# Kernel optimization log

Hardware: AMD Instinct MI355X
Metric: run time of the kernel (lower is better)

Reference implementation:

```python
import jax, jax.numpy as jnp
import numpy as np

# YOLOv3 anchors (9 pairs, 3 per scale), matching init_kwargs
ANCHORS = np.array([[10,13],[16,30],[33,23],[30,61],[62,45],[59,119],[116,90],[156,198],[373,326]], dtype=np.float32)
B, C = 3, 20
IGNORE_THRESH = 0.7


def iou_xywh(a, b):
    """IoU of boxes in (cx,cy,w,h); a,b broadcastable [...,4]."""
    ax1, ax2 = a[..., 0] - a[..., 2] * 0.5, a[..., 0] + a[..., 2] * 0.5
    ay1, ay2 = a[..., 1] - a[..., 3] * 0.5, a[..., 1] + a[..., 3] * 0.5
    bx1, bx2 = b[..., 0] - b[..., 2] * 0.5, b[..., 0] + b[..., 2] * 0.5
    by1, by2 = b[..., 1] - b[..., 3] * 0.5, b[..., 1] + b[..., 3] * 0.5
    iw = jnp.clip(jnp.minimum(ax2, bx2) - jnp.maximum(ax1, bx1), 0.0)
    ih = jnp.clip(jnp.minimum(ay2, by2) - jnp.maximum(ay1, by1), 0.0)
    inter = iw * ih
    union = a[..., 2] * a[..., 3] + b[..., 2] * b[..., 3] - inter
    return inter / (union + 1e-16)


def _scale_loss(pred, targets, idx, img_size):
    anchors_total = jnp.asarray(ANCHORS)                      # [9,2]
    N = pred.shape[0]
    g = pred.shape[2]
    p = pred.reshape(N, B, C + 5, g, g).transpose(0, 1, 3, 4, 2)  # [N,B,g,g,C+5]
    xy = jax.nn.sigmoid(p[..., 0:2])
    wh = p[..., 2:4]                                          # raw tw,th
    conf = jax.nn.sigmoid(p[..., 4])
    pcls = jax.nn.sigmoid(p[..., 5:])

    yv, xv = jnp.meshgrid(jnp.arange(g), jnp.arange(g), indexing='ij')
    grid = jnp.stack([xv, yv], -1).astype(pred.dtype)[None, None]  # [1,1,g,g,2]
    a_wh = anchors_total[idx * B:(idx + 1) * B].reshape(1, B, 1, 1, 2)
    preds_coords = jnp.concatenate([(xy + grid) / g, jnp.exp(wh) * a_wh / img_size], -1)  # [N,B,g,g,4]

    tcls = targets[..., 0].astype(jnp.int32)                  # [N,T]
    tb = targets[..., 1:]                                     # [N,T,4]
    # break-on-first-zero-x semantics
    valid = jnp.cumprod((tb[..., 0] != 0).astype(jnp.int32), axis=1).astype(bool)

    # noobj mask: max IoU of every pred box vs every valid target
    ious = iou_xywh(preds_coords[:, None], tb[:, :, None, None, None])  # [N,T,B,g,g]
    ious = jnp.where(valid[:, :, None, None, None], ious, -1.0)
    noobj = ious.max(axis=1) <= IGNORE_THRESH                 # [N,B,g,g]

    # best-anchor matching (shift both to origin: only w,h matter)
    anc4 = jnp.concatenate([jnp.zeros_like(anchors_total), anchors_total / img_size], -1)  # [9,4]
    tb0 = tb.at[..., 0:2].set(0.0)
    a_ious = iou_xywh(anc4[None, None], tb0[:, :, None])      # [N,T,9]
    k = jnp.argmax(a_ious, axis=-1)                           # [N,T] global anchor idx
    matched = valid & (k // B == idx)
    local = k % B
    ii = jnp.clip(jnp.floor(tb[..., 0] * g), 0, g - 1).astype(jnp.int32)
    jj = jnp.clip(jnp.floor(tb[..., 1] * g), 0, g - 1).astype(jnp.int32)

    kwh = anchors_total[k]                                    # [N,T,2]
    tw_safe = jnp.maximum(tb[..., 2], 1e-12)                  # guard log(0) for padded rows (dropped anyway)
    th_safe = jnp.maximum(tb[..., 3], 1e-12)
    enc = jnp.stack([tb[..., 0] * g - ii,
                     tb[..., 1] * g - jj,
                     jnp.log(tw_safe * img_size / kwh[..., 0]),
                     jnp.log(th_safe * img_size / kwh[..., 1])], -1)  # [N,T,4]
    scale4 = jnp.broadcast_to((2.0 - tb[..., 2] * tb[..., 3])[..., None], enc.shape)

    b_idx = jnp.broadcast_to(jnp.arange(N)[:, None], matched.shape)
    b_s = jnp.where(matched, b_idx, N)                        # OOB batch idx -> dropped by scatter
    obj = jnp.zeros((N, B, g, g), bool).at[b_s, local, jj, ii].set(True, mode='drop')
    noobj = noobj.at[b_s, local, jj, ii].set(False, mode='drop')
    cls_t = jnp.zeros((N, B, g, g, C), pred.dtype).at[b_s, local, jj, ii, tcls].set(1.0, mode='drop')
    enc_t = jnp.zeros((N, B, g, g, 4), pred.dtype).at[b_s, local, jj, ii].set(enc, mode='drop')
    scl_t = jnp.zeros((N, B, g, g, 4), pred.dtype).at[b_s, local, jj, ii].set(scale4, mode='drop')

    loss_noobj = jnp.sum(jnp.where(noobj, conf, 0.0) ** 2)
    loss_obj = jnp.sum(jnp.where(obj, conf - 1.0, 0.0) ** 2)
    loss_class = jnp.sum(jnp.where(obj[..., None], pcls - cls_t, 0.0) ** 2)
    raw4 = jnp.concatenate([xy, wh], -1)
    diff = (raw4 - enc_t) * scl_t
    loss_coords = jnp.sum(jnp.where(obj[..., None], diff, 0.0) ** 2)
    return (loss_class + loss_obj + loss_noobj + loss_coords) / N


def setup_inputs() -> dict:
    key = jax.random.key(0)
    k0, k1, k2, k3, k4, k5, k6 = jax.random.split(key, 7)
    N, T = 16, 40
    pred0 = jax.random.normal(k0, (N, B * (C + 5), 19, 19), jnp.float32) * 0.5
    pred1 = jax.random.normal(k1, (N, B * (C + 5), 38, 38), jnp.float32) * 0.5
    pred2 = jax.random.normal(k2, (N, B * (C + 5), 76, 76), jnp.float32) * 0.5
    cls = jax.random.randint(k3, (N, T, 1), 0, C).astype(jnp.float32)
    xy = jax.random.uniform(k4, (N, T, 2), minval=0.05, maxval=0.95)
    wh = jax.random.uniform(k5, (N, T, 2), minval=0.02, maxval=0.4)
    counts = jax.random.randint(k6, (N, 1), 5, T + 1)
    mask = (jnp.arange(T)[None, :] < counts).astype(jnp.float32)[..., None]
    targets = jnp.concatenate([cls, xy, wh], -1) * mask  # zero padding tail -> break semantics
    return {"pred0": pred0, "pred1": pred1, "pred2": pred2, "targets": targets, "img_size": 608}


def reference(pred0, pred1, pred2, targets, img_size):
    return (_scale_loss(pred0, targets, 0, img_size)
            + _scale_loss(pred1, targets, 1, img_size)
            + _scale_loss(pred2, targets, 2, img_size))
```

## Files before the change

### kernel.cpp

```cpp
#include <hip/hip_runtime.h>

#define NB 16
#define TT 40
#define BA 3
#define CC 20

__constant__ float cANCH[18] = {10,13, 16,30, 33,23, 30,61, 62,45,
                                59,119, 116,90, 156,198, 373,326};

__device__ __forceinline__ float sigmoidf_(float x){ return 1.f/(1.f+__expf(-x)); }

__global__ __launch_bounds__(256) void yolo_loss_33457795236259_kernel(
    const float* __restrict__ p0, const float* __restrict__ p1,
    const float* __restrict__ p2, const float* __restrict__ targets,
    const void* __restrict__ imgp, float* __restrict__ out)
{
  const int n  = blockIdx.y;
  const int bx = blockIdx.x;
  int s, g, cellbase;
  const float* pred;
  if (bx < 5)       { s = 0; g = 19; pred = p0; cellbase = bx * 256; }
  else if (bx < 22) { s = 1; g = 38; pred = p1; cellbase = (bx - 5) * 256; }
  else              { s = 2; g = 76; pred = p2; cellbase = (bx - 22) * 256; }

  __shared__ float stx1[TT], stx2[TT], sty1[TT], sty2[TT], sarea[TT];
  __shared__ float senc0[TT], senc1[TT], senc2[TT], senc3[TT], sscl[TT];
  __shared__ int   smkey[TT];
  __shared__ int   scount;
  __shared__ float swsum[4];

  float img;
  { int v = *(const int*)imgp;
    img = (v >= 1 && v <= 1000000) ? (float)v : *(const float*)imgp; }

  const int tid = threadIdx.x;
  if (tid < TT) {
    const int t = tid;
    const float* tg = targets + (n * TT + t) * 5;
    float tcf = tg[0];
    float tx = tg[1], ty = tg[2], tw = tg[3], th = tg[4];
    bool valid = true;
    for (int u = 0; u <= t; ++u)
      if (targets[(n * TT + u) * 5 + 1] == 0.f) { valid = false; break; }
    stx1[t] = tx - tw * 0.5f; stx2[t] = tx + tw * 0.5f;
    sty1[t] = ty - th * 0.5f; sty2[t] = ty + th * 0.5f;
    sarea[t] = tw * th;
    sscl[t]  = 2.f - tw * th;
    int k = 0; float best = -1.f;
    for (int a = 0; a < 9; ++a) {
      float aw = cANCH[2*a] / img, ah = cANCH[2*a+1] / img;
      float inter = fminf(aw, tw) * fminf(ah, th);
      float uni   = aw * ah + tw * th - inter;
      float iou   = inter / (uni + 1e-16f);
      if (iou > best) { best = iou; k = a; }
    }
    float gf = (float)g;
    int ii = (int)floorf(tx * gf); ii = ii < 0 ? 0 : (ii > g-1 ? g-1 : ii);
    int jj = (int)floorf(ty * gf); jj = jj < 0 ? 0 : (jj > g-1 ? g-1 : jj);
    bool m = valid && (k / BA == s);
    int kl = k % BA;
    int tc = (int)tcf;
    smkey[t] = m ? (ii | (jj << 7) | (kl << 14) | (tc << 16)) : -1;
    senc0[t] = tx * gf - (float)ii;
    senc1[t] = ty * gf - (float)jj;
    senc2[t] = __logf(fmaxf(tw, 1e-12f) * img / cANCH[2*k]);
    senc3[t] = __logf(fmaxf(th, 1e-12f) * img / cANCH[2*k+1]);
    if (t == 0) {
      int cnt = 0;
      while (cnt < TT && targets[(n * TT + cnt) * 5 + 1] != 0.f) cnt++;
      scount = cnt;
    }
  }
  __syncthreads();

  float partial = 0.f;
  const int gg = g * g;
  const int cell = cellbase + tid;
  if (cell < BA * gg) {
    int b = cell / gg;
    int rem = cell - b * gg;
    int i = rem / g;
    int j = rem - i * g;
    const float* pc = pred + ((size_t)(n * BA + b) * (CC + 5)) * gg + rem;
    float rx = pc[0];
    float ry = pc[(size_t)gg];
    float rw = pc[(size_t)2 * gg];
    float rh = pc[(size_t)3 * gg];
    float rconf = pc[(size_t)4 * gg];
    float sx = sigmoidf_(rx), sy = sigmoidf_(ry), conf = sigmoidf_(rconf);
    float aw = cANCH[2*(s*BA+b)] / img, ah = cANCH[2*(s*BA+b)+1] / img;
    float pw = __expf(rw) * aw, ph = __expf(rh) * ah;
    float gf = (float)g;
    float cx = (sx + (float)j) / gf, cy = (sy + (float)i) / gf;
    float px1 = cx - pw * 0.5f, px2 = cx + pw * 0.5f;
    float py1 = cy - ph * 0.5f, py2 = cy + ph * 0.5f;
    float areaP = pw * ph;
    float maxiou = -1.f;
    int win = -1; unsigned clsmask = 0u;
    int mykey = j | (i << 7) | (b << 14);
    int cnt = scount;
    for (int t = 0; t < cnt; ++t) {
      float iw = fminf(px2, stx2[t]) - fmaxf(px1, stx1[t]);
      float ih = fminf(py2, sty2[t]) - fmaxf(py1, sty1[t]);
      iw = fmaxf(iw, 0.f); ih = fmaxf(ih, 0.f);
      float inter = iw * ih;
      float iou = inter / (areaP + sarea[t] - inter + 1e-16f);
      maxiou = fmaxf(maxiou, iou);
      int mk = smkey[t];
      if ((mk & 0xFFFF) == mykey) { win = t; clsmask |= 1u << (mk >> 16); }
    }
    if (win >= 0) {
      float d = conf - 1.f; partial += d * d;
      float scl = sscl[win];
      float d0 = (sx - senc0[win]) * scl;
      float d1 = (sy - senc1[win]) * scl;
      float d2 = (rw - senc2[win]) * scl;
      float d3 = (rh - senc3[win]) * scl;
      partial += d0*d0 + d1*d1 + d2*d2 + d3*d3;
      #pragma unroll
      for (int c = 0; c < CC; ++c) {
        float pcl = sigmoidf_(pc[(size_t)(5 + c) * gg]);
        float tv = ((clsmask >> c) & 1u) ? 1.f : 0.f;
        float dd = pcl - tv;
        partial += dd * dd;
      }
    } else if (maxiou <= 0.7f) {
      partial += conf * conf;
    }
  }

  #pragma unroll
  for (int o = 32; o >= 1; o >>= 1) partial += __shfl_down(partial, o, 64);
  int lane = tid & 63, wid = tid >> 6;
  if (lane == 0) swsum[wid] = partial;
  __syncthreads();
  if (tid == 0) {
    atomicAdd(out, (swsum[0] + swsum[1] + swsum[2] + swsum[3]) * (1.f / (float)NB));
  }
}

extern "C" void kernel_launch(void* const* d_in, const int* in_sizes, int n_in,
                              void* d_out, int out_size, void* d_ws, size_t ws_size,
                              hipStream_t stream) {
  const float* p0 = (const float*)d_in[0];
  const float* p1 = (const float*)d_in[1];
  const float* p2 = (const float*)d_in[2];
  const float* tg = (const float*)d_in[3];
  const void*  im = d_in[4];
  float* out = (float*)d_out;

  hipMemsetAsync(out, 0, sizeof(float), stream);

  dim3 grid(90, NB);
  yolo_loss_33457795236259_kernel<<<grid, 256, 0, stream>>>(p0, p1, p2, tg, im, out);
}
```

Before: 107.6 us.

## Replace atomic accumulation with per-block partials and a separate reduce kernel

Each block now writes its partial sum into a workspace array instead of doing an atomicAdd to the output, and a second single-block kernel reduces the partials. This drops the memset and the atomics and makes the sum deterministic, at the cost of an extra kernel launch. Target data in shared memory is packed into float4/float2 structs so the IoU loop issues fewer LDS instructions. The per-thread prefix validity scan is replaced by a single count computed before the target setup.

After: 102.1 us. -5.1%, faster.

```diff
diff --git a/kernel.cpp b/kernel.cpp
--- a/kernel.cpp
+++ b/kernel.cpp
@@ -4,16 +4,17 @@
 #define TT 40
 #define BA 3
 #define CC 20
+#define GX 90
 
 __constant__ float cANCH[18] = {10,13, 16,30, 33,23, 30,61, 62,45,
                                 59,119, 116,90, 156,198, 373,326};
 
 __device__ __forceinline__ float sigmoidf_(float x){ return 1.f/(1.f+__expf(-x)); }
 
-__global__ __launch_bounds__(256) void yolo_loss_33457795236259_kernel(
+__global__ __launch_bounds__(256) void yolo_part_kernel(
     const float* __restrict__ p0, const float* __restrict__ p1,
     const float* __restrict__ p2, const float* __restrict__ targets,
-    const void* __restrict__ imgp, float* __restrict__ out)
+    const void* __restrict__ imgp, float* __restrict__ partials)
 {
   const int n  = blockIdx.y;
   const int bx = blockIdx.x;
@@ -23,29 +24,33 @@
   else if (bx < 22) { s = 1; g = 38; pred = p1; cellbase = (bx - 5) * 256; }
   else              { s = 2; g = 76; pred = p2; cellbase = (bx - 22) * 256; }
 
-  __shared__ float stx1[TT], stx2[TT], sty1[TT], sty2[TT], sarea[TT];
-  __shared__ float senc0[TT], senc1[TT], senc2[TT], senc3[TT], sscl[TT];
-  __shared__ int   smkey[TT];
-  __shared__ int   scount;
-  __shared__ float swsum[4];
+  __shared__ float4 sbox[TT];
+  __shared__ float2 sai[TT];
+  __shared__ float4 sencv[TT];
+  __shared__ float  sscl[TT];
+  __shared__ int    scount;
+  __shared__ float  swsum[4];
 
   float img;
   { int v = *(const int*)imgp;
     img = (v >= 1 && v <= 1000000) ? (float)v : *(const float*)imgp; }
 
   const int tid = threadIdx.x;
+  if (tid == 0) {
+    int cnt = 0;
+    while (cnt < TT && targets[(n * TT + cnt) * 5 + 1] != 0.f) cnt++;
+    scount = cnt;
+  }
+  __syncthreads();
   if (tid < TT) {
     const int t = tid;
     const float* tg = targets + (n * TT + t) * 5;
     float tcf = tg[0];
     float tx = tg[1], ty = tg[2], tw = tg[3], th = tg[4];
-    bool valid = true;
-    for (int u = 0; u <= t; ++u)
-      if (targets[(n * TT + u) * 5 + 1] == 0.f) { valid = false; break; }
-    stx1[t] = tx - tw * 0.5f; stx2[t] = tx + tw * 0.5f;
-    sty1[t] = ty - th * 0.5f; sty2[t] = ty + th * 0.5f;
-    sarea[t] = tw * th;
-    sscl[t]  = 2.f - tw * th;
+    bool valid = t < scount;
+    sbox[t] = make_float4(tx - tw * 0.5f, tx + tw * 0.5f,
+                          ty - th * 0.5f, ty + th * 0.5f);
+    sscl[t] = 2.f - tw * th;
     int k = 0; float best = -1.f;
     for (int a = 0; a < 9; ++a) {
       float aw = cANCH[2*a] / img, ah = cANCH[2*a+1] / img;
@@ -60,16 +65,11 @@
     bool m = valid && (k / BA == s);
     int kl = k % BA;
     int tc = (int)tcf;
-    smkey[t] = m ? (ii | (jj << 7) | (kl << 14) | (tc << 16)) : -1;
-    senc0[t] = tx * gf - (float)ii;
-    senc1[t] = ty * gf - (float)jj;
-    senc2[t] = __logf(fmaxf(tw, 1e-12f) * img / cANCH[2*k]);
-    senc3[t] = __logf(fmaxf(th, 1e-12f) * img / cANCH[2*k+1]);
-    if (t == 0) {
-      int cnt = 0;
-      while (cnt < TT && targets[(n * TT + cnt) * 5 + 1] != 0.f) cnt++;
-      scount = cnt;
-    }
+    int key = m ? (ii | (jj << 7) | (kl << 14) | (tc << 16)) : -1;
+    sai[t] = make_float2(tw * th, __int_as_float(key));
+    sencv[t] = make_float4(tx * gf - (float)ii, ty * gf - (float)jj,
+                           __logf(fmaxf(tw, 1e-12f) * img / cANCH[2*k]),
+                           __logf(fmaxf(th, 1e-12f) * img / cANCH[2*k+1]));
   }
   __syncthreads();
 
@@ -100,22 +100,25 @@
     int mykey = j | (i << 7) | (b << 14);
     int cnt = scount;
     for (int t = 0; t < cnt; ++t) {
-      float iw = fminf(px2, stx2[t]) - fmaxf(px1, stx1[t]);
-      float ih = fminf(py2, sty2[t]) - fmaxf(py1, sty1[t]);
+      float4 bb = sbox[t];
+      float2 am = sai[t];
+      float iw = fminf(px2, bb.y) - fmaxf(px1, bb.x);
+      float ih = fminf(py2, bb.w) - fmaxf(py1, bb.z);
       iw = fmaxf(iw, 0.f); ih = fmaxf(ih, 0.f);
       float inter = iw * ih;
-      float iou = inter / (areaP + sarea[t] - inter + 1e-16f);
+      float iou = inter / (areaP + am.x - inter + 1e-16f);
       maxiou = fmaxf(maxiou, iou);
-      int mk = smkey[t];
+      int mk = __float_as_int(am.y);
       if ((mk & 0xFFFF) == mykey) { win = t; clsmask |= 1u << (mk >> 16); }
     }
     if (win >= 0) {
       float d = conf - 1.f; partial += d * d;
       float scl = sscl[win];
-      float d0 = (sx - senc0[win]) * scl;
-      float d1 = (sy - senc1[win]) * scl;
-      float d2 = (rw - senc2[win]) * scl;
-      float d3 = (rh - senc3[win]) * scl;
+      float4 e = sencv[win];
+      float d0 = (sx - e.x) * scl;
+      float d1 = (sy - e.y) * scl;
+      float d2 = (rw - e.z) * scl;
+      float d3 = (rh - e.w) * scl;
       partial += d0*d0 + d1*d1 + d2*d2 + d3*d3;
       #pragma unroll
       for (int c = 0; c < CC; ++c) {
@@ -134,9 +137,23 @@
   int lane = tid & 63, wid = tid >> 6;
   if (lane == 0) swsum[wid] = partial;
   __syncthreads();
-  if (tid == 0) {
-    atomicAdd(out, (swsum[0] + swsum[1] + swsum[2] + swsum[3]) * (1.f / (float)NB));
-  }
+  if (tid == 0)
+    partials[n * GX + bx] = swsum[0] + swsum[1] + swsum[2] + swsum[3];
+}
+
+__global__ __launch_bounds__(256) void yolo_reduce_kernel(
+    const float* __restrict__ partials, float* __restrict__ out)
+{
+  const int tid = threadIdx.x;
+  float v = 0.f;
+  for (int idx = tid; idx < NB * GX; idx += 256) v += partials[idx];
+  #pragma unroll
+  for (int o = 32; o >= 1; o >>= 1) v += __shfl_down(v, o, 64);
+  __shared__ float swsum[4];
+  if ((tid & 63) == 0) swsum[tid >> 6] = v;
+  __syncthreads();
+  if (tid == 0)
+    out[0] = (swsum[0] + swsum[1] + swsum[2] + swsum[3]) * (1.f / (float)NB);
 }
 
 extern "C" void kernel_launch(void* const* d_in, const int* in_sizes, int n_in,
@@ -148,9 +165,9 @@
   const float* tg = (const float*)d_in[3];
   const void*  im = d_in[4];
   float* out = (float*)d_out;
+  float* partials = (float*)d_ws;
 
-  hipMemsetAsync(out, 0, sizeof(float), stream);
-
-  dim3 grid(90, NB);
-  yolo_loss_33457795236259_kernel<<<grid, 256, 0, stream>>>(p0, p1, p2, tg, im, out);
+  dim3 grid(GX, NB);
+  yolo_part_kernel<<<grid, 256, 0, stream>>>(p0, p1, p2, tg, im, partials);
+  yolo_reduce_kernel<<<1, 256, 0, stream>>>(partials, out);
 }
```
